# Kernel tuning notes

Hardware: AMD Instinct MI355X
Metric: run time of the kernel (lower is better)

The kernel has to match this reference:

```python
import jax, jax.numpy as jnp
import numpy as np

M, TX, N_A, N_VALUES = 4096, 128, 512, 256
W_SCALE = 0.05  # keep gates in non-saturated range through 128 recurrent steps


def setup_inputs() -> dict:
    key = jax.random.key(0)
    ks = jax.random.split(key, 4)
    X = jax.random.normal(ks[0], (M, TX, N_VALUES), dtype=jnp.float32)
    a0 = jnp.zeros((M, N_A), dtype=jnp.float32)
    c0 = jnp.zeros((M, N_A), dtype=jnp.float32)
    # PyTorch LSTM params, gate order (i, f, g, o) stacked along dim 0
    W_ih = jax.random.normal(ks[1], (4 * N_A, N_VALUES), dtype=jnp.float32) * W_SCALE
    W_hh = jax.random.normal(ks[2], (4 * N_A, N_A), dtype=jnp.float32) * W_SCALE
    b_ih = jnp.zeros((4 * N_A,), dtype=jnp.float32)
    b_hh = jnp.zeros((4 * N_A,), dtype=jnp.float32)
    W_out = jax.random.normal(ks[3], (N_VALUES, N_A), dtype=jnp.float32) * W_SCALE
    b_out = jnp.zeros((N_VALUES,), dtype=jnp.float32)
    return {"X": X, "a0": a0, "c0": c0, "W_ih": W_ih, "W_hh": W_hh,
            "b_ih": b_ih, "b_hh": b_hh, "W_out": W_out, "b_out": b_out}


def reference(X, a0, c0, W_ih, W_hh, b_ih, b_hh, W_out, b_out):
    # One LSTM cell step + Linear projection per timestep (PyTorch gate order i,f,g,o).
    b = b_ih + b_hh

    def step(carry, x_t):
        h, c = carry
        gates = x_t @ W_ih.T + h @ W_hh.T + b  # [m, 4*n_a]
        i, f, g, o = jnp.split(gates, 4, axis=-1)
        c_new = jax.nn.sigmoid(f) * c + jax.nn.sigmoid(i) * jnp.tanh(g)
        h_new = jax.nn.sigmoid(o) * jnp.tanh(c_new)
        out = h_new @ W_out.T + b_out  # [m, n_values]
        return (h_new, c_new), out

    xs = jnp.swapaxes(X, 0, 1)  # [Tx, m, n_values] for scan over time
    (_, _), outs = jax.lax.scan(step, (a0, c0), xs)
    return outs  # [Tx, m, n_values] == stacked list of per-step outputs
```

## Files before the change

kernel.cpp:

```cpp
#include <hip/hip_runtime.h>
#include <math.h>

typedef _Float16 f16;
typedef _Float16 f16x8 __attribute__((ext_vector_type(8)));
typedef float f32x4 __attribute__((ext_vector_type(4)));
typedef unsigned int u32;
typedef unsigned short u16;

#define M_DIM 4096
#define T_X   128
#define NV    256
#define NA    512
#define NG    2048
#define NKT   24

__device__ __forceinline__ float sigf(float x) { return 1.0f / (1.0f + __expf(-x)); }
__device__ __forceinline__ float tanh_fast(float x) {
    float t = __expf(2.0f * x);
    return (t - 1.0f) / (t + 1.0f);
}

#define GLOAD_LDS16(G, L) \
    __builtin_amdgcn_global_load_lds((const __attribute__((address_space(1))) u32*)(G), \
                                     (__attribute__((address_space(3))) u32*)(L), 16, 0, 0)

__global__ void prep(const float* __restrict__ X,
                     const float* __restrict__ a0, const float* __restrict__ c0,
                     const float* __restrict__ W_ih, const float* __restrict__ W_hh,
                     const float* __restrict__ b_ih, const float* __restrict__ b_hh,
                     const float* __restrict__ W_out,
                     u16* __restrict__ Ha, float* __restrict__ cws,
                     u16* __restrict__ BG, u16* __restrict__ BOs, u16* __restrict__ BOo,
                     float* __restrict__ bs, u16* __restrict__ Xf)
{
    const int N_BG  = NKT * 16 * 4096;
    const int N_BOS = 16 * 16 * 512;
    const int N_BOO = 16 * 4 * 2048;
    const int N_BS  = NG;
    const int N_H   = 32 * 16 * 4096;
    const int N_XF  = 2 * 32 * 8 * 4096;
    const int N_C   = M_DIM * NA;
    const int NT = N_BG + N_BOS + N_BOO + N_BS + N_H + N_XF + N_C;
    for (int idx = blockIdx.x * blockDim.x + threadIdx.x; idx < NT;
         idx += gridDim.x * blockDim.x) {
        int i = idx;
        if (i < N_BG) {
            int tile = i >> 12, w = i & 4095;
            int jb = tile & 15, kt = tile >> 4;
            int f = w >> 9, lane = (w >> 3) & 63, e = w & 7;
            int wcc = f >> 2, g = f & 3;
            int n = g * NA + jb * 32 + wcc * 16 + (lane & 15);
            int k = kt * 32 + ((lane >> 4) << 3) + e;
            float v = (k < NV) ? W_ih[n * NV + k] : W_hh[n * NA + (k - NV)];
            BG[i] = __builtin_bit_cast(u16, (f16)v);
            continue;
        }
        i -= N_BG;
        if (i < N_BOS) {
            int tile = i >> 9, w = i & 511;
            int s = tile & 15, kt = tile >> 4;
            int lane = w >> 3, e = w & 7;
            int n = s * 16 + (lane & 15);
            int k = kt * 32 + ((lane >> 4) << 3) + e;
            BOs[i] = __builtin_bit_cast(u16, (f16)W_out[n * NA + k]);
            continue;
        }
        i -= N_BOS;
        if (i < N_BOO) {
            int tile = i >> 11, w = i & 2047;
            int nb = tile & 3, kt = tile >> 2;
            int f = w >> 9, lane = (w >> 3) & 63, e = w & 7;
            int n = nb * 64 + f * 16 + (lane & 15);
            int k = kt * 32 + ((lane >> 4) << 3) + e;
            BOo[i] = __builtin_bit_cast(u16, (f16)W_out[n * NA + k]);
            continue;
        }
        i -= N_BOO;
        if (i < N_BS) { bs[i] = b_ih[i] + b_hh[i]; continue; }
        i -= N_BS;
        if (i < N_H) {
            int tile = i >> 12, w = i & 4095;
            int kt = tile & 15, mb = tile >> 4;
            int mf = w >> 9, lane = (w >> 3) & 63, e = w & 7;
            int m = mb * 128 + mf * 16 + (lane & 15);
            int k = kt * 32 + ((lane >> 4) << 3) + e;
            Ha[i] = __builtin_bit_cast(u16, (f16)a0[m * NA + k]);
            continue;
        }
        i -= N_H;
        if (i < N_XF) {
            int b = i >> 20, j = i & 1048575;
            int tile = j >> 12, w = j & 4095;
            int kt = tile & 7, mb = tile >> 3;
            int mf = w >> 9, lane = (w >> 3) & 63, e = w & 7;
            int m = mb * 128 + mf * 16 + (lane & 15);
            int k = kt * 32 + ((lane >> 4) << 3) + e;
            Xf[i] = __builtin_bit_cast(u16, (f16)X[(size_t)m * (T_X * NV) + b * NV + k]);
            continue;
        }
        i -= N_XF;
        {
            int id  = i >> 12;
            int rem = i & 4095;
            int tid = rem >> 4, r16 = rem & 15;
            int fm = r16 >> 2, q = r16 & 3;
            int xcd = id & 7, g2 = id >> 3;
            int jb = g2 & 15, mb = xcd + 8 * (g2 >> 4);
            int lane = tid & 63, wv = tid >> 6;
            int wr = wv >> 1, wc = wv & 1;
            int ll = lane & 15, lh = lane >> 4;
            int m = mb * 128 + (wr * 4 + fm) * 16 + lh * 4 + q;
            int col = jb * 32 + wc * 16 + ll;
            cws[i] = c0[(size_t)m * NA + col];
        }
    }
}

__global__ __launch_bounds__(256, 2)
void step_fused(const float* __restrict__ X,
                const u16* __restrict__ Xf_cur, u16* __restrict__ Xf_n2,
                const u16* __restrict__ Hin, u16* __restrict__ Hout,
                float* __restrict__ cws,
                const u16* __restrict__ BG, const u16* __restrict__ BOs,
                const float* __restrict__ bs, const float* __restrict__ b_out,
                float* __restrict__ out_prev, int t, int do_out, int do_xconv)
{
    __shared__ char smem[65536];
    char* BO_lds = smem + 49152;

    const int id  = blockIdx.x;
    const int xcd = id & 7, g2 = id >> 3;
    const int jb  = g2 & 15;
    const int mb  = xcd + 8 * (g2 >> 4);

    const int tid = threadIdx.x, lane = tid & 63, wv = tid >> 6;
    const int wr = wv >> 1, wc = wv & 1;

    f32x4 cv4[4];
    {
        const f32x4* cb = (const f32x4*)(cws + ((size_t)id * 256 + tid) * 16);
        #pragma unroll
        for (int i = 0; i < 4; ++i) cv4[i] = __builtin_nontemporal_load(cb + i);
    }
    asm volatile("s_waitcnt vmcnt(0)" ::: "memory");

    f32x4 acc[4][4];
    #pragma unroll
    for (int a = 0; a < 4; ++a)
        #pragma unroll
        for (int b = 0; b < 4; ++b) acc[a][b] = (f32x4){0.f, 0.f, 0.f, 0.f};
    f32x4 acc_o[4];
    #pragma unroll
    for (int a = 0; a < 4; ++a) acc_o[a] = (f32x4){0.f, 0.f, 0.f, 0.f};

    auto stage = [&](int ktn, int buf) {
        char* base = smem + buf * 16384;
        const char* asrc = (ktn < 8)
            ? (const char*)(Xf_cur + ((size_t)(mb * 8 + ktn)) * 4096)
            : (const char*)(Hin + ((size_t)(mb * 16 + (ktn - 8))) * 4096);
        GLOAD_LDS16(asrc + wv * 2048 + lane * 16,        base + wv * 2048);
        GLOAD_LDS16(asrc + wv * 2048 + 1024 + lane * 16, base + wv * 2048 + 1024);
        const char* bsrc = (const char*)(BG + ((size_t)(ktn * 16 + jb)) * 4096);
        GLOAD_LDS16(bsrc + wv * 2048 + lane * 16,        base + 8192 + wv * 2048);
        GLOAD_LDS16(bsrc + wv * 2048 + 1024 + lane * 16, base + 8192 + wv * 2048 + 1024);
    };
    auto compute = [&](int ktn, int buf) {
        const char* base = smem + buf * 16384;
        f16x8 af[4], bfr[4];
        #pragma unroll
        for (int g = 0; g < 4; ++g)
            bfr[g] = *(const f16x8*)(base + 8192 + (((wc * 4 + g) * 64 + lane) << 4));
        #pragma unroll
        for (int fm = 0; fm < 4; ++fm)
            af[fm] = *(const f16x8*)(base + (((wr * 4 + fm) * 64 + lane) << 4));
        #pragma unroll
        for (int fm = 0; fm < 4; ++fm)
            #pragma unroll
            for (int g = 0; g < 4; ++g)
                acc[fm][g] = __builtin_amdgcn_mfma_f32_16x16x32_f16(af[fm], bfr[g], acc[fm][g], 0, 0, 0);
        if (do_out && ktn >= 8 && ((ktn - 8) & 1) == wc) {
            f16x8 bo = *(const f16x8*)(BO_lds + (ktn - 8) * 1024 + lane * 16);
            #pragma unroll
            for (int fm = 0; fm < 4; ++fm)
                acc_o[fm] = __builtin_amdgcn_mfma_f32_16x16x32_f16(af[fm], bo, acc_o[fm], 0, 0, 0);
        }
    };

    #pragma unroll
    for (int i = 0; i < 4; ++i) {
        int kt = wv * 4 + i;
        const char* src = (const char*)(BOs + ((size_t)(kt * 16 + jb)) * 512);
        GLOAD_LDS16(src + lane * 16, BO_lds + kt * 1024);
    }
    stage(0, 0);
    stage(1, 1);

    int cur = 0;
    for (int kt = 0; kt < NKT - 1; ++kt) {
        asm volatile("s_waitcnt vmcnt(4)" ::: "memory");
        __builtin_amdgcn_s_barrier();
        if (kt + 2 < NKT) {
            int stb = cur + 2; if (stb >= 3) stb -= 3;
            stage(kt + 2, stb);
        }
        compute(kt, cur);
        ++cur; if (cur == 3) cur = 0;
    }
    asm volatile("s_waitcnt vmcnt(0)" ::: "memory");
    __builtin_amdgcn_s_barrier();
    compute(NKT - 1, cur);

    const int ll = lane & 15, lh = lane >> 4;
    const int colg = jb * 32 + wc * 16 + ll;
    float bsv[4];
    #pragma unroll
    for (int g = 0; g < 4; ++g) bsv[g] = bs[g * NA + colg];

    u16* htile = Hout + ((size_t)(mb * 16 + jb)) * 4096;
    const int ksub = wc * 2 + (ll >> 3);
    const int e = ll & 7;

    #pragma unroll
    for (int fm = 0; fm < 4; ++fm) {
        const int mf = wr * 4 + fm;
        #pragma unroll
        for (int q = 0; q < 4; ++q) {
            float gi = acc[fm][0][q] + bsv[0];
            float gf = acc[fm][1][q] + bsv[1];
            float gg = acc[fm][2][q] + bsv[2];
            float go = acc[fm][3][q] + bsv[3];
            float iv = sigf(gi), fv = sigf(gf);
            float gv = tanh_fast(gg), ov = sigf(go);
            float cn = fv * cv4[fm][q] + iv * gv;
            float hn = ov * tanh_fast(cn);
            cv4[fm][q] = cn;
            const int lanep = (lh * 4 + q) + 16 * ksub;
            htile[(mf * 64 + lanep) * 8 + e] = __builtin_bit_cast(u16, (f16)hn);
        }
    }
    {
        f32x4* cb = (f32x4*)(cws + ((size_t)id * 256 + tid) * 16);
        #pragma unroll
        for (int i = 0; i < 4; ++i) __builtin_nontemporal_store(cv4[i], cb + i);
    }

    if (do_out) {
        if (wc == 1) {
            float* P = (float*)(smem + wr * 4096);
            #pragma unroll
            for (int fm = 0; fm < 4; ++fm)
                #pragma unroll
                for (int q = 0; q < 4; ++q)
                    P[(fm * 16 + lh * 4 + q) * 16 + ll] = acc_o[fm][q];
        }
        __syncthreads();
        if (wc == 0) {
            const float* P = (const float*)(smem + wr * 4096);
            const float bo = b_out[jb * 16 + ll];
            #pragma unroll
            for (int fm = 0; fm < 4; ++fm)
                #pragma unroll
                for (int q = 0; q < 4; ++q) {
                    const int rloc = wr * 64 + fm * 16 + lh * 4 + q;
                    float v = acc_o[fm][q] + P[(fm * 16 + lh * 4 + q) * 16 + ll] + bo;
                    __builtin_nontemporal_store(
                        v, out_prev + ((size_t)mb * 128 + rloc) * NV + jb * 16 + ll);
                }
        }
    }

    if (do_xconv && jb < 8) {
        const int r = tid >> 1, kh = tid & 1;
        const float* xsrc = X + ((size_t)(mb * 128 + r) * T_X + (t + 2)) * NV + jb * 32 + kh * 16;
        f32x4 xv[4];
        #pragma unroll
        for (int i = 0; i < 4; ++i)
            xv[i] = __builtin_nontemporal_load((const f32x4*)(xsrc + i * 4));
        u16* xt = Xf_n2 + ((size_t)(mb * 8 + jb)) * 4096;
        const int mf = r >> 4;
        #pragma unroll
        for (int s = 0; s < 2; ++s) {
            f16x8 v;
            #pragma unroll
            for (int j = 0; j < 8; ++j) v[j] = (f16)xv[s * 2 + (j >> 2)][j & 3];
            const int lanep = (r & 15) + 16 * (kh * 2 + s);
            *(f16x8*)(xt + (mf * 64 + lanep) * 8) = v;
        }
    }
}

__global__ __launch_bounds__(256)
void out_proj(const u16* __restrict__ Hin, const u16* __restrict__ BO,
              const float* __restrict__ b_out, float* __restrict__ out)
{
    __shared__ char smem[24576];

    const int id  = blockIdx.x;
    const int xcd = id & 7, g2 = id >> 3;
    const int nb  = g2 & 3;
    const int mb  = xcd + 8 * (g2 >> 2);

    const int tid = threadIdx.x, lane = tid & 63, wv = tid >> 6;
    const int wr = wv >> 1, wc = wv & 1;

    f32x4 acc[4][2];
    #pragma unroll
    for (int a = 0; a < 4; ++a) { acc[a][0] = (f32x4){0,0,0,0}; acc[a][1] = (f32x4){0,0,0,0}; }

    auto stage = [&](int kt, int buf) {
        char* base = smem + buf * 12288;
        const char* asrc = (const char*)(Hin + ((size_t)(mb * 16 + kt)) * 4096);
        GLOAD_LDS16(asrc + wv * 2048 + lane * 16,        base + wv * 2048);
        GLOAD_LDS16(asrc + wv * 2048 + 1024 + lane * 16, base + wv * 2048 + 1024);
        const char* bsrc = (const char*)(BO + ((size_t)(kt * 4 + nb)) * 2048);
        GLOAD_LDS16(bsrc + wv * 1024 + lane * 16, base + 8192 + wv * 1024);
    };
    auto compute = [&](int buf) {
        const char* base = smem + buf * 12288;
        f16x8 bfr[2];
        #pragma unroll
        for (int fq = 0; fq < 2; ++fq)
            bfr[fq] = *(const f16x8*)(base + 8192 + (((wc * 2 + fq) * 64 + lane) << 4));
        #pragma unroll
        for (int fm = 0; fm < 4; ++fm) {
            f16x8 af = *(const f16x8*)(base + (((wr * 4 + fm) * 64 + lane) << 4));
            #pragma unroll
            for (int fq = 0; fq < 2; ++fq)
                acc[fm][fq] = __builtin_amdgcn_mfma_f32_16x16x32_f16(af, bfr[fq], acc[fm][fq], 0, 0, 0);
        }
    };

    stage(0, 0);
    __syncthreads();
    for (int kt = 0; kt < 16; ++kt) {
        const int cur = kt & 1;
        if (kt + 1 < 16) stage(kt + 1, cur ^ 1);
        compute(cur);
        __syncthreads();
    }

    const int ll = lane & 15, lh = lane >> 4;
    float bov[2];
    #pragma unroll
    for (int fq = 0; fq < 2; ++fq) bov[fq] = b_out[nb * 64 + (wc * 2 + fq) * 16 + ll];

    #pragma unroll
    for (int fm = 0; fm < 4; ++fm)
        #pragma unroll
        for (int fq = 0; fq < 2; ++fq)
            #pragma unroll
            for (int q = 0; q < 4; ++q) {
                const int row = mb * 128 + wr * 64 + fm * 16 + lh * 4 + q;
                const int col = nb * 64 + (wc * 2 + fq) * 16 + ll;
                __builtin_nontemporal_store(acc[fm][fq][q] + bov[fq],
                                            out + (size_t)row * NV + col);
            }
}

extern "C" void kernel_launch(void* const* d_in, const int* in_sizes, int n_in,
                              void* d_out, int out_size, void* d_ws, size_t ws_size,
                              hipStream_t stream) {
    const float* X     = (const float*)d_in[0];
    const float* a0    = (const float*)d_in[1];
    const float* c0    = (const float*)d_in[2];
    const float* W_ih  = (const float*)d_in[3];
    const float* W_hh  = (const float*)d_in[4];
    const float* b_ih  = (const float*)d_in[5];
    const float* b_hh  = (const float*)d_in[6];
    const float* W_out = (const float*)d_in[7];
    const float* b_out = (const float*)d_in[8];
    float* out = (float*)d_out;

    char* w = (char*)d_ws;
    u16*   Ha   = (u16*)(w);
    u16*   Hb   = (u16*)(w + ((size_t)4 << 20));
    float* cws  = (float*)(w + ((size_t)8 << 20));
    u16*   BG   = (u16*)(w + ((size_t)16 << 20));
    u16*   BOs  = (u16*)(w + ((size_t)19 << 20));
    u16*   BOo  = (u16*)(w + ((size_t)19 << 20) + 262144);
    float* bsv  = (float*)(w + ((size_t)19 << 20) + 524288);
    u16*   Xf   = (u16*)(w + ((size_t)20 << 20));

    prep<<<8192, 256, 0, stream>>>(X, a0, c0, W_ih, W_hh, b_ih, b_hh, W_out,
                                   Ha, cws, BG, BOs, BOo, bsv, Xf);

    for (int t = 0; t < T_X; ++t) {
        const u16* hi = (t & 1) ? Hb : Ha;
        u16*       ho = (t & 1) ? Ha : Hb;
        const u16* xc = Xf + (size_t)(t % 3) * 1048576;
        u16*       xn = Xf + (size_t)((t + 2) % 3) * 1048576;
        float* outp = out + (size_t)(t > 0 ? t - 1 : 0) * M_DIM * NV;
        step_fused<<<512, 256, 0, stream>>>(X, xc, xn, hi, ho, cws, BG, BOs, bsv, b_out,
                                            outp, t, t > 0 ? 1 : 0, t < T_X - 2 ? 1 : 0);
    }
    out_proj<<<128, 256, 0, stream>>>(Ha, BOo, b_out, out + (size_t)(T_X - 1) * M_DIM * NV);
}
```

Measured before the change: 3.951 ms.

## Split step tile across eight waves instead of four per block

The fused LSTM step kernel now runs 512 threads (8 waves) per block. Each wave computes a 32-row slice instead of 64 rows, which halves accumulators, per-wave staging loads and the stored cell-state slice, and the workspace layout for c is remapped to match. The cell-state load moves from before the GEMM loop to after it, and plain loads and stores replace the nontemporal ones. This aims for more waves in flight per CU to hide latency, at the cost of less B-fragment reuse per wave and more LDS read traffic per MFMA.

```diff
diff --git a/kernel.cpp b/kernel.cpp
--- a/kernel.cpp
+++ b/kernel.cpp
@@ -29,7 +29,7 @@
                      const float* __restrict__ W_ih, const float* __restrict__ W_hh,
                      const float* __restrict__ b_ih, const float* __restrict__ b_hh,
                      const float* __restrict__ W_out,
-                     u16* __restrict__ Ha, float* __restrict__ cws,
+                     u16* __restrict__ H0, float* __restrict__ cws,
                      u16* __restrict__ BG, u16* __restrict__ BOs, u16* __restrict__ BOo,
                      float* __restrict__ bs, u16* __restrict__ Xf)
 {
@@ -84,7 +84,7 @@
             int mf = w >> 9, lane = (w >> 3) & 63, e = w & 7;
             int m = mb * 128 + mf * 16 + (lane & 15);
             int k = kt * 32 + ((lane >> 4) << 3) + e;
-            Ha[i] = __builtin_bit_cast(u16, (f16)a0[m * NA + k]);
+            H0[i] = __builtin_bit_cast(u16, (f16)a0[m * NA + k]);
             continue;
         }
         i -= N_H;
@@ -102,21 +102,21 @@
         {
             int id  = i >> 12;
             int rem = i & 4095;
-            int tid = rem >> 4, r16 = rem & 15;
-            int fm = r16 >> 2, q = r16 & 3;
+            int tid = rem >> 3, r8 = rem & 7;
+            int fm = r8 >> 2, q = r8 & 3;
             int xcd = id & 7, g2 = id >> 3;
             int jb = g2 & 15, mb = xcd + 8 * (g2 >> 4);
             int lane = tid & 63, wv = tid >> 6;
             int wr = wv >> 1, wc = wv & 1;
             int ll = lane & 15, lh = lane >> 4;
-            int m = mb * 128 + (wr * 4 + fm) * 16 + lh * 4 + q;
+            int m = mb * 128 + (wr * 2 + fm) * 16 + lh * 4 + q;
             int col = jb * 32 + wc * 16 + ll;
             cws[i] = c0[(size_t)m * NA + col];
         }
     }
 }
 
-__global__ __launch_bounds__(256, 2)
+__global__ __launch_bounds__(512, 4)
 void step_fused(const float* __restrict__ X,
                 const u16* __restrict__ Xf_cur, u16* __restrict__ Xf_n2,
                 const u16* __restrict__ Hin, u16* __restrict__ Hout,
@@ -136,59 +136,49 @@
     const int tid = threadIdx.x, lane = tid & 63, wv = tid >> 6;
     const int wr = wv >> 1, wc = wv & 1;
 
-    f32x4 cv4[4];
-    {
-        const f32x4* cb = (const f32x4*)(cws + ((size_t)id * 256 + tid) * 16);
-        #pragma unroll
-        for (int i = 0; i < 4; ++i) cv4[i] = __builtin_nontemporal_load(cb + i);
-    }
-    asm volatile("s_waitcnt vmcnt(0)" ::: "memory");
-
-    f32x4 acc[4][4];
-    #pragma unroll
-    for (int a = 0; a < 4; ++a)
+    f32x4 acc[2][4];
+    #pragma unroll
+    for (int a = 0; a < 2; ++a)
         #pragma unroll
         for (int b = 0; b < 4; ++b) acc[a][b] = (f32x4){0.f, 0.f, 0.f, 0.f};
-    f32x4 acc_o[4];
-    #pragma unroll
-    for (int a = 0; a < 4; ++a) acc_o[a] = (f32x4){0.f, 0.f, 0.f, 0.f};
+    f32x4 acc_o[2];
+    acc_o[0] = (f32x4){0.f, 0.f, 0.f, 0.f};
+    acc_o[1] = (f32x4){0.f, 0.f, 0.f, 0.f};
 
     auto stage = [&](int ktn, int buf) {
         char* base = smem + buf * 16384;
         const char* asrc = (ktn < 8)
             ? (const char*)(Xf_cur + ((size_t)(mb * 8 + ktn)) * 4096)
             : (const char*)(Hin + ((size_t)(mb * 16 + (ktn - 8))) * 4096);
-        GLOAD_LDS16(asrc + wv * 2048 + lane * 16,        base + wv * 2048);
-        GLOAD_LDS16(asrc + wv * 2048 + 1024 + lane * 16, base + wv * 2048 + 1024);
+        GLOAD_LDS16(asrc + wv * 1024 + lane * 16, base + wv * 1024);
         const char* bsrc = (const char*)(BG + ((size_t)(ktn * 16 + jb)) * 4096);
-        GLOAD_LDS16(bsrc + wv * 2048 + lane * 16,        base + 8192 + wv * 2048);
-        GLOAD_LDS16(bsrc + wv * 2048 + 1024 + lane * 16, base + 8192 + wv * 2048 + 1024);
+        GLOAD_LDS16(bsrc + wv * 1024 + lane * 16, base + 8192 + wv * 1024);
     };
     auto compute = [&](int ktn, int buf) {
         const char* base = smem + buf * 16384;
-        f16x8 af[4], bfr[4];
+        f16x8 af[2], bfr[4];
         #pragma unroll
         for (int g = 0; g < 4; ++g)
             bfr[g] = *(const f16x8*)(base + 8192 + (((wc * 4 + g) * 64 + lane) << 4));
         #pragma unroll
-        for (int fm = 0; fm < 4; ++fm)
-            af[fm] = *(const f16x8*)(base + (((wr * 4 + fm) * 64 + lane) << 4));
-        #pragma unroll
-        for (int fm = 0; fm < 4; ++fm)
+        for (int fm = 0; fm < 2; ++fm)
+            af[fm] = *(const f16x8*)(base + (((wr * 2 + fm) * 64 + lane) << 4));
+        #pragma unroll
+        for (int fm = 0; fm < 2; ++fm)
             #pragma unroll
             for (int g = 0; g < 4; ++g)
                 acc[fm][g] = __builtin_amdgcn_mfma_f32_16x16x32_f16(af[fm], bfr[g], acc[fm][g], 0, 0, 0);
         if (do_out && ktn >= 8 && ((ktn - 8) & 1) == wc) {
             f16x8 bo = *(const f16x8*)(BO_lds + (ktn - 8) * 1024 + lane * 16);
             #pragma unroll
-            for (int fm = 0; fm < 4; ++fm)
+            for (int fm = 0; fm < 2; ++fm)
                 acc_o[fm] = __builtin_amdgcn_mfma_f32_16x16x32_f16(af[fm], bo, acc_o[fm], 0, 0, 0);
         }
     };
 
     #pragma unroll
-    for (int i = 0; i < 4; ++i) {
-        int kt = wv * 4 + i;
+    for (int i = 0; i < 2; ++i) {
+        int kt = wv * 2 + i;
         const char* src = (const char*)(BOs + ((size_t)(kt * 16 + jb)) * 512);
         GLOAD_LDS16(src + lane * 16, BO_lds + kt * 1024);
     }
@@ -197,7 +187,7 @@
 
     int cur = 0;
     for (int kt = 0; kt < NKT - 1; ++kt) {
-        asm volatile("s_waitcnt vmcnt(4)" ::: "memory");
+        asm volatile("s_waitcnt vmcnt(2)" ::: "memory");
         __builtin_amdgcn_s_barrier();
         if (kt + 2 < NKT) {
             int stb = cur + 2; if (stb >= 3) stb -= 3;
@@ -215,14 +205,19 @@
     float bsv[4];
     #pragma unroll
     for (int g = 0; g < 4; ++g) bsv[g] = bs[g * NA + colg];
+    f32x4 cv4[2];
+    {
+        const f32x4* cb = (const f32x4*)(cws + ((size_t)id * 512 + tid) * 8);
+        cv4[0] = cb[0]; cv4[1] = cb[1];
+    }
 
     u16* htile = Hout + ((size_t)(mb * 16 + jb)) * 4096;
     const int ksub = wc * 2 + (ll >> 3);
     const int e = ll & 7;
 
     #pragma unroll
-    for (int fm = 0; fm < 4; ++fm) {
-        const int mf = wr * 4 + fm;
+    for (int fm = 0; fm < 2; ++fm) {
+        const int mf = wr * 2 + fm;
         #pragma unroll
         for (int q = 0; q < 4; ++q) {
             float gi = acc[fm][0][q] + bsv[0];
@@ -239,29 +234,28 @@
         }
     }
     {
-        f32x4* cb = (f32x4*)(cws + ((size_t)id * 256 + tid) * 16);
-        #pragma unroll
-        for (int i = 0; i < 4; ++i) __builtin_nontemporal_store(cv4[i], cb + i);
+        f32x4* cb = (f32x4*)(cws + ((size_t)id * 512 + tid) * 8);
+        cb[0] = cv4[0]; cb[1] = cv4[1];
     }
 
     if (do_out) {
         if (wc == 1) {
-            float* P = (float*)(smem + wr * 4096);
-            #pragma unroll
-            for (int fm = 0; fm < 4; ++fm)
+            float* P = (float*)(smem + wr * 2048);
+            #pragma unroll
+            for (int fm = 0; fm < 2; ++fm)
                 #pragma unroll
                 for (int q = 0; q < 4; ++q)
                     P[(fm * 16 + lh * 4 + q) * 16 + ll] = acc_o[fm][q];
         }
         __syncthreads();
         if (wc == 0) {
-            const float* P = (const float*)(smem + wr * 4096);
+            const float* P = (const float*)(smem + wr * 2048);
             const float bo = b_out[jb * 16 + ll];
             #pragma unroll
-            for (int fm = 0; fm < 4; ++fm)
+            for (int fm = 0; fm < 2; ++fm)
                 #pragma unroll
                 for (int q = 0; q < 4; ++q) {
-                    const int rloc = wr * 64 + fm * 16 + lh * 4 + q;
+                    const int rloc = wr * 32 + fm * 16 + lh * 4 + q;
                     float v = acc_o[fm][q] + P[(fm * 16 + lh * 4 + q) * 16 + ll] + bo;
                     __builtin_nontemporal_store(
                         v, out_prev + ((size_t)mb * 128 + rloc) * NV + jb * 16 + ll);
@@ -270,22 +264,17 @@
     }
 
     if (do_xconv && jb < 8) {
-        const int r = tid >> 1, kh = tid & 1;
-        const float* xsrc = X + ((size_t)(mb * 128 + r) * T_X + (t + 2)) * NV + jb * 32 + kh * 16;
-        f32x4 xv[4];
-        #pragma unroll
-        for (int i = 0; i < 4; ++i)
-            xv[i] = __builtin_nontemporal_load((const f32x4*)(xsrc + i * 4));
+        const int r = tid >> 2, kq = tid & 3;
+        const float* xsrc = X + ((size_t)(mb * 128 + r) * T_X + (t + 2)) * NV + jb * 32 + kq * 8;
+        f32x4 xv0 = __builtin_nontemporal_load((const f32x4*)xsrc);
+        f32x4 xv1 = __builtin_nontemporal_load((const f32x4*)(xsrc + 4));
+        f16x8 v;
+        #pragma unroll
+        for (int j = 0; j < 4; ++j) { v[j] = (f16)xv0[j]; v[4 + j] = (f16)xv1[j]; }
         u16* xt = Xf_n2 + ((size_t)(mb * 8 + jb)) * 4096;
         const int mf = r >> 4;
-        #pragma unroll
-        for (int s = 0; s < 2; ++s) {
-            f16x8 v;
-            #pragma unroll
-            for (int j = 0; j < 8; ++j) v[j] = (f16)xv[s * 2 + (j >> 2)][j & 3];
-            const int lanep = (r & 15) + 16 * (kh * 2 + s);
-            *(f16x8*)(xt + (mf * 64 + lanep) * 8) = v;
-        }
+        const int lanep = (r & 15) + 16 * kq;
+        *(f16x8*)(xt + (mf * 64 + lanep) * 8) = v;
     }
 }
 
@@ -372,8 +361,8 @@
     float* out = (float*)d_out;
 
     char* w = (char*)d_ws;
-    u16*   Ha   = (u16*)(w);
-    u16*   Hb   = (u16*)(w + ((size_t)4 << 20));
+    u16*   H0   = (u16*)(w);
+    u16*   H1   = (u16*)(w + ((size_t)4 << 20));
     float* cws  = (float*)(w + ((size_t)8 << 20));
     u16*   BG   = (u16*)(w + ((size_t)16 << 20));
     u16*   BOs  = (u16*)(w + ((size_t)19 << 20));
@@ -382,16 +371,16 @@
     u16*   Xf   = (u16*)(w + ((size_t)20 << 20));
 
     prep<<<8192, 256, 0, stream>>>(X, a0, c0, W_ih, W_hh, b_ih, b_hh, W_out,
-                                   Ha, cws, BG, BOs, BOo, bsv, Xf);
+                                   H0, cws, BG, BOs, BOo, bsv, Xf);
 
     for (int t = 0; t < T_X; ++t) {
-        const u16* hi = (t & 1) ? Hb : Ha;
-        u16*       ho = (t & 1) ? Ha : Hb;
+        const u16* hi = (t & 1) ? H1 : H0;
+        u16*       ho = (t & 1) ? H0 : H1;
         const u16* xc = Xf + (size_t)(t % 3) * 1048576;
         u16*       xn = Xf + (size_t)((t + 2) % 3) * 1048576;
         float* outp = out + (size_t)(t > 0 ? t - 1 : 0) * M_DIM * NV;
-        step_fused<<<512, 256, 0, stream>>>(X, xc, xn, hi, ho, cws, BG, BOs, bsv, b_out,
+        step_fused<<<512, 512, 0, stream>>>(X, xc, xn, hi, ho, cws, BG, BOs, bsv, b_out,
                                             outp, t, t > 0 ? 1 : 0, t < T_X - 2 ? 1 : 0);
     }
-    out_proj<<<128, 256, 0, stream>>>(Ha, BOo, b_out, out + (size_t)(T_X - 1) * M_DIM * NV);
-}
+    out_proj<<<128, 256, 0, stream>>>(H0, BOo, b_out, out + (size_t)(T_X - 1) * M_DIM * NV);
+}
```

New measurement: 3.448 ms. 1.15x faster.
